# Performance work log

Measured on AMD Instinct MI355X. Metric: run time of the kernel, lower is better.

Reference implementation:

```python
import jax, jax.numpy as jnp
import numpy as np
from functools import partial

DIM, HID, DK, NH, SEQ, B = 1024, 512, 512, 4, 16, 2048
DH = DK // NH  # per-head dim = 128
EPS = 1e-5


def _ln(x, g, b):
    m = x.mean(-1, keepdims=True)
    v = ((x - m) ** 2).mean(-1, keepdims=True)
    return (x - m) * jax.lax.rsqrt(v + EPS) * g + b


def setup_inputs() -> dict:
    key = jax.random.key(0)
    ks = jax.random.split(key, 32)
    it = iter(range(32))
    n = lambda shape, s: jax.random.normal(ks[next(it)], shape, jnp.float32) * s
    inp = {
        'visual': n((B, SEQ, DIM), 1.0),
        'text':   n((B, SEQ, DIM), 1.0),
        'user':   n((B, SEQ, DIM), 1.0),
        'cat':    n((B, SEQ, DIM), 1.0),
        'label':  n((B, SEQ, 1), 1.0),
        'h0':     n((B, HID), 1.0),
        'c0':     n((B, HID), 1.0),
        # fusion MLP: Linear(4*dim -> dim)
        'fus_W': n((DIM, 4 * DIM), 1.0 / np.sqrt(4 * DIM)),
        'fus_b': n((DIM,), 0.01),
        # LayerNormLSTM cell params (gate order i,f,g,o)
        'W_ih': n((4 * HID, DIM), 1.0 / np.sqrt(DIM)),
        'W_hh': n((4 * HID, HID), 1.0 / np.sqrt(HID)),
        'g_ih': 1.0 + n((4 * HID,), 0.1), 'b_ih': n((4 * HID,), 0.01),
        'g_hh': 1.0 + n((4 * HID,), 0.1), 'b_hh': n((4 * HID,), 0.01),
        'g_c':  1.0 + n((HID,), 0.1),     'b_c':  n((HID,), 0.01),
        # attention projections
        'wq_W': n((DK, HID), 1.0 / np.sqrt(HID)), 'wq_b': n((DK,), 0.01),
        'wk_W': n((DK, HID), 1.0 / np.sqrt(HID)), 'wk_b': n((DK,), 0.01),
        'wv_W': n((NH, DK, HID), 1.0 / np.sqrt(HID)), 'wv_b': n((NH, DK), 0.01),
        'wout_W': n((DK, DK * NH), 1.0 / np.sqrt(DK * NH)), 'wout_b': n((DK,), 0.01),
        'out_W': n((1, DK), 1.0 / np.sqrt(DK)), 'out_b': n((1,), 0.01),
    }
    return inp


def reference(visual, text, user, cat, label, h0, c0, fus_W, fus_b,
              W_ih, W_hh, g_ih, b_ih, g_hh, b_hh, g_c, b_c,
              wq_W, wq_b, wk_W, wk_b, wv_W, wv_b, wout_W, wout_b, out_W, out_b):
    # fusion MLP (dropout is identity at inference)
    mods = jnp.concatenate([visual, text, user, cat], axis=-1)  # [B,S,4*DIM]
    v_t = jax.nn.relu(mods @ fus_W.T + fus_b)                    # [B,S,DIM]

    # LayerNorm-LSTM recurrence over time via scan
    def step(carry, x_t):
        h, c = carry
        gates = _ln(x_t @ W_ih.T, g_ih, b_ih) + _ln(h @ W_hh.T, g_hh, b_hh)
        i, f, g, o = jnp.split(gates, 4, axis=-1)
        c = jax.nn.sigmoid(f) * c + jax.nn.sigmoid(i) * jnp.tanh(g)
        h = jax.nn.sigmoid(o) * jnp.tanh(_ln(c, g_c, b_c))
        return (h, c), h

    (hn, _), hs = jax.lax.scan(step, (h0, c0), jnp.swapaxes(v_t, 0, 1))
    lstm_out = jnp.swapaxes(hs, 0, 1)  # [B,S,HID]

    # multi-head dot self-attention against final hidden state
    q = (hn @ wq_W.T + wq_b).reshape(-1, NH, DH)                    # [B,H,dh]
    k = (lstm_out @ wk_W.T + wk_b).reshape(-1, SEQ, NH, DH)         # [B,S,H,dh]
    scores = jnp.einsum('bshd,bhd->bhs', k, q) / np.sqrt(DH)        # [B,H,S]
    attn = jax.nn.softmax(scores, axis=-1)
    # per-head full-width values: V[b,h,s,k]
    V = jnp.einsum('hkd,bsd->bhsk', wv_W, lstm_out) + wv_b[None, :, None, :]
    ctx = jnp.einsum('bhsk,bhs->bhk', V, attn).reshape(-1, NH * DK)  # [B,H*DK]
    out_h = ctx @ wout_W.T + wout_b                                  # [B,DK]
    output = out_h @ out_W.T + out_b                                 # [B,1]

    label_one = label[:, -1, 0]
    loss = jnp.mean((output.reshape(-1) - label_one) ** 2)
    return loss, output
```

## Files before the change

### kernel.cpp

```cpp
#include <hip/hip_runtime.h>
#include <cstdint>

#define B_SZ 2048
#define SEQ  16
#define DIM  1024
#define HID  512
#define DK   512
#define NH   4
#define DH   128
#define GATE 2048
#define EPSV 1e-5f

typedef __bf16 bf8_t __attribute__((ext_vector_type(8)));
typedef float  f4_t  __attribute__((ext_vector_type(4)));
typedef unsigned short u16x8 __attribute__((ext_vector_type(8)));
typedef unsigned short u16x4 __attribute__((ext_vector_type(4)));

__device__ __forceinline__ unsigned short f2bf(float f){
  __bf16 h = (__bf16)f;
  return __builtin_bit_cast(unsigned short, h);
}
__device__ __forceinline__ float bf2f(unsigned short u){
  return __builtin_bit_cast(float, ((unsigned int)u) << 16);
}
__device__ __forceinline__ float sigm(float x){ return 1.f/(1.f+__expf(-x)); }
__device__ __forceinline__ float tanh_f(float x){ return 1.f - 2.f/(__expf(2.f*x)+1.f); }

__device__ __forceinline__ void gload16(const void* g, void* l){
  __builtin_amdgcn_global_load_lds(
      (const __attribute__((address_space(1))) void*)g,
      (__attribute__((address_space(3))) void*)l, 16, 0, 0);
}

template<bool OUT_BF16, bool BIAS, bool RELU>
__global__ __launch_bounds__(512, 1) void gemm8p(
    const unsigned short* __restrict__ A,
    const unsigned short* __restrict__ Bw,
    const float* __restrict__ bias,
    void* __restrict__ Cp,
    int N, int K, int nwg)
{
  __shared__ __align__(16) unsigned short As[2][256*64];
  __shared__ __align__(16) unsigned short Bs[2][256*64];
  const int tid = threadIdx.x, lane = tid & 63, w = tid >> 6;
  const int bid = blockIdx.x;
  const int swz = (bid & 7)*(nwg >> 3) + (bid >> 3);
  const int nx  = N >> 8;
  const int lnx = 31 - __clz(nx);
  const int bm0 = (swz >> lnx) << 8;
  const int bn0 = (swz & (nx-1)) << 8;

  const int l8  = lane >> 3;
  const int gsw = (lane & 7) ^ l8;
  const int fr  = lane & 15, kg = lane >> 4;
  const int wm  = (w >> 2)*128, wn = (w & 3)*64;
  const int KT  = K >> 6;

  auto stA = [&](int buf, int kt, int h){
    #pragma unroll
    for (int c=0;c<2;++c){
      const int rb = h*128 + c*64 + w*8;
      gload16(A + (size_t)(bm0 + rb + l8)*K + (size_t)kt*64 + gsw*8, &As[buf][rb*64]);
    }
  };
  auto stB = [&](int buf, int kt, int h){
    #pragma unroll
    for (int c=0;c<2;++c){
      const int rb = h*128 + c*64 + w*8;
      gload16(Bw + (size_t)(bn0 + rb + l8)*K + (size_t)kt*64 + gsw*8, &Bs[buf][rb*64]);
    }
  };
  auto rdA = [&](int buf, int m, int kk)->bf8_t{
    return *(const bf8_t*)&As[buf][(wm + m*16 + fr)*64 + (((kk*4+kg) ^ (fr&7))*8)];
  };
  auto rdB = [&](int buf, int n, int kk)->bf8_t{
    return *(const bf8_t*)&Bs[buf][(wn + n*16 + fr)*64 + (((kk*4+kg) ^ (fr&7))*8)];
  };

  f4_t acc[8][4];
  #pragma unroll
  for (int m=0;m<8;++m)
    #pragma unroll
    for (int n=0;n<4;++n) acc[m][n] = (f4_t)0.f;

  bf8_t bfr[4][2];

  auto mfma2 = [&](int m0, const bf8_t a00, const bf8_t a01,
                   const bf8_t a10, const bf8_t a11){
    __builtin_amdgcn_s_setprio(1);
    #pragma unroll
    for (int n=0;n<4;++n){
      acc[m0][n]   = __builtin_amdgcn_mfma_f32_16x16x32_bf16(a00, bfr[n][0], acc[m0][n],   0,0,0);
      acc[m0][n]   = __builtin_amdgcn_mfma_f32_16x16x32_bf16(a01, bfr[n][1], acc[m0][n],   0,0,0);
      acc[m0+1][n] = __builtin_amdgcn_mfma_f32_16x16x32_bf16(a10, bfr[n][0], acc[m0+1][n], 0,0,0);
      acc[m0+1][n] = __builtin_amdgcn_mfma_f32_16x16x32_bf16(a11, bfr[n][1], acc[m0+1][n], 0,0,0);
    }
    __builtin_amdgcn_s_setprio(0);
  };

  auto phase12 = [&](int buf, auto&& stg){
    #pragma unroll
    for (int n=0;n<4;++n){ bfr[n][0]=rdB(buf,n,0); bfr[n][1]=rdB(buf,n,1); }
    const bf8_t a00=rdA(buf,0,0), a01=rdA(buf,0,1), a10=rdA(buf,1,0), a11=rdA(buf,1,1);
    stg();
    asm volatile("s_barrier" ::: "memory");
    mfma2(0, a00,a01,a10,a11);
    asm volatile("s_barrier" ::: "memory");
  };
  auto phase4 = [&](int buf, int m0, auto&& stg, bool vm){
    const bf8_t a00=rdA(buf,m0,0), a01=rdA(buf,m0,1), a10=rdA(buf,m0+1,0), a11=rdA(buf,m0+1,1);
    stg();
    if (vm){
      __builtin_amdgcn_sched_barrier(0);
      asm volatile("s_waitcnt vmcnt(4)" ::: "memory");
    }
    asm volatile("s_barrier" ::: "memory");
    mfma2(m0, a00,a01,a10,a11);
    asm volatile("s_barrier" ::: "memory");
  };

  stA(0,0,0); stA(0,0,1); stB(0,0,0); stB(0,0,1);
  stB(1,1,0); stB(1,1,1);
  __builtin_amdgcn_sched_barrier(0);
  asm volatile("s_waitcnt vmcnt(4)" ::: "memory");
  asm volatile("s_barrier" ::: "memory");

  const int NIT = KT >> 1;
  for (int it=0; it<NIT; ++it){
    const int t0 = 2*it, t1 = t0+1;
    const int tN  = (t0+2 < KT) ? t0+2 : KT-1;
    const int tB3 = (t1+2 < KT) ? t1+2 : KT-1;

    phase12(0,      [&]{ stA(1,t1,0);  });
    phase4 (0, 2,   [&]{ stA(1,t1,1);  }, false);
    phase4 (0, 4,   [&]{ stB(0,tN,0);  }, false);
    phase4 (0, 6,   [&]{ stB(0,tN,1);  }, true);
    phase12(1,      [&]{ stA(0,tN,0);  });
    phase4 (1, 2,   [&]{ stA(0,tN,1);  }, false);
    phase4 (1, 4,   [&]{ stB(1,tB3,0); }, false);
    phase4 (1, 6,   [&]{ stB(1,tB3,1); }, true);
  }

  #pragma unroll
  for (int n=0;n<4;++n){
    const int col = bn0 + wn + n*16 + fr;
    float bv = 0.f;
    if constexpr (BIAS) bv = bias[col];
    #pragma unroll
    for (int m=0;m<8;++m){
      #pragma unroll
      for (int j=0;j<4;++j){
        const int row = bm0 + wm + m*16 + kg*4 + j;
        float v = acc[m][n][j] + bv;
        if constexpr (RELU) v = fmaxf(v, 0.f);
        if constexpr (OUT_BF16) ((unsigned short*)Cp)[(size_t)row*N + col] = f2bf(v);
        else                    ((float*)Cp)[(size_t)row*N + col] = v;
      }
    }
  }
}

__global__ __launch_bounds__(512, 1) void gemm8pf(
    const float* __restrict__ A0, const float* __restrict__ A1,
    const float* __restrict__ A2, const float* __restrict__ A3,
    const unsigned short* __restrict__ Bw,
    const float* __restrict__ bias,
    unsigned short* __restrict__ Cp,
    int N, int K, int nwg)
{
  __shared__ __align__(16) unsigned short As[2][256*64];
  __shared__ __align__(16) unsigned short Bs[2][256*64];
  const int tid = threadIdx.x, lane = tid & 63, w = tid >> 6;
  const int bid = blockIdx.x;
  const int swz = (bid & 7)*(nwg >> 3) + (bid >> 3);
  const int nx  = N >> 8;
  const int lnx = 31 - __clz(nx);
  const int bm0 = (swz >> lnx) << 8;
  const int bn0 = (swz & (nx-1)) << 8;

  const int l8  = lane >> 3;
  const int gsw = (lane & 7) ^ l8;
  const int fr  = lane & 15, kg = lane >> 4;
  const int wm  = (w >> 2)*128, wn = (w & 3)*64;
  const int KT  = K >> 6;

  auto stB = [&](int buf, int kt, int h){
    #pragma unroll
    for (int c=0;c<2;++c){
      const int rb = h*128 + c*64 + w*8;
      gload16(Bw + (size_t)(bn0 + rb + l8)*K + (size_t)kt*64 + gsw*8, &Bs[buf][rb*64]);
    }
  };

  f4_t rg0[2], rg1[2], rg2[2], rg3[2];
  auto ldQ = [&](f4_t* rg, int kt, int q){
    const int kb = kt*64, si = kb >> 10, kc = kb & 1023;
    const float* Asel = si==0?A0 : si==1?A1 : si==2?A2 : A3;
    const float* p = Asel + (size_t)(bm0 + q*64 + (tid>>3))*1024 + kc + (tid&7)*8;
    rg[0] = *(const f4_t*)p; rg[1] = *(const f4_t*)(p+4);
  };
  auto wrQ = [&](const f4_t* rg, int buf, int q){
    const int R = q*64 + (tid>>3);
    const int g = (tid&7) ^ (R&7);
    u16x8 wv;
    #pragma unroll
    for (int j=0;j<4;++j){ wv[j]=f2bf(rg[0][j]); wv[4+j]=f2bf(rg[1][j]); }
    *(u16x8*)&As[buf][R*64 + g*8] = wv;
  };

  auto rdA = [&](int buf, int m, int kk)->bf8_t{
    return *(const bf8_t*)&As[buf][(wm + m*16 + fr)*64 + (((kk*4+kg) ^ (fr&7))*8)];
  };
  auto rdB = [&](int buf, int n, int kk)->bf8_t{
    return *(const bf8_t*)&Bs[buf][(wn + n*16 + fr)*64 + (((kk*4+kg) ^ (fr&7))*8)];
  };

  f4_t acc[8][4];
  #pragma unroll
  for (int m=0;m<8;++m)
    #pragma unroll
    for (int n=0;n<4;++n) acc[m][n] = (f4_t)0.f;

  bf8_t bfr[4][2];

  auto mfma2 = [&](int m0, const bf8_t a00, const bf8_t a01,
                   const bf8_t a10, const bf8_t a11){
    __builtin_amdgcn_s_setprio(1);
    #pragma unroll
    for (int n=0;n<4;++n){
      acc[m0][n]   = __builtin_amdgcn_mfma_f32_16x16x32_bf16(a00, bfr[n][0], acc[m0][n],   0,0,0);
      acc[m0][n]   = __builtin_amdgcn_mfma_f32_16x16x32_bf16(a01, bfr[n][1], acc[m0][n],   0,0,0);
      acc[m0+1][n] = __builtin_amdgcn_mfma_f32_16x16x32_bf16(a10, bfr[n][0], acc[m0+1][n], 0,0,0);
      acc[m0+1][n] = __builtin_amdgcn_mfma_f32_16x16x32_bf16(a11, bfr[n][1], acc[m0+1][n], 0,0,0);
    }
    __builtin_amdgcn_s_setprio(0);
  };

  auto phase12 = [&](int buf, auto&& stg){
    #pragma unroll
    for (int n=0;n<4;++n){ bfr[n][0]=rdB(buf,n,0); bfr[n][1]=rdB(buf,n,1); }
    const bf8_t a00=rdA(buf,0,0), a01=rdA(buf,0,1), a10=rdA(buf,1,0), a11=rdA(buf,1,1);
    stg();
    asm volatile("s_barrier" ::: "memory");
    mfma2(0, a00,a01,a10,a11);
    asm volatile("s_barrier" ::: "memory");
  };
  auto phase4 = [&](int buf, int m0, auto&& stg){
    const bf8_t a00=rdA(buf,m0,0), a01=rdA(buf,m0,1), a10=rdA(buf,m0+1,0), a11=rdA(buf,m0+1,1);
    stg();
    asm volatile("s_barrier" ::: "memory");
    mfma2(m0, a00,a01,a10,a11);
    asm volatile("s_barrier" ::: "memory");
  };

  stB(0,0,0); stB(0,0,1); stB(1,1,0); stB(1,1,1);
  ldQ(rg0,0,0); ldQ(rg1,0,1); ldQ(rg2,0,2); ldQ(rg3,0,3);
  wrQ(rg0,0,0); wrQ(rg1,0,1); wrQ(rg2,0,2); wrQ(rg3,0,3);
  __builtin_amdgcn_sched_barrier(0);
  ldQ(rg0,1,0); ldQ(rg1,1,1); ldQ(rg2,1,2); ldQ(rg3,1,3);
  asm volatile("s_waitcnt lgkmcnt(0)" ::: "memory");
  asm volatile("s_barrier" ::: "memory");

  const int NIT = KT >> 1;
  for (int it=0; it<NIT; ++it){
    const int t1  = 2*it+1;
    const int tN  = (t1+1 < KT) ? t1+1 : KT-1;
    const int tB3 = (t1+2 < KT) ? t1+2 : KT-1;

    phase12(0, [&]{ wrQ(rg0,1,0); __builtin_amdgcn_sched_barrier(0); ldQ(rg0,tN,0); });
    phase4 (0, 2, [&]{ wrQ(rg1,1,1); __builtin_amdgcn_sched_barrier(0); ldQ(rg1,tN,1); });
    phase4 (0, 4, [&]{ wrQ(rg2,1,2); stB(0,tN,0);
                       __builtin_amdgcn_sched_barrier(0); ldQ(rg2,tN,2); });
    phase4 (0, 6, [&]{ wrQ(rg3,1,3); stB(0,tN,1);
                       __builtin_amdgcn_sched_barrier(0); ldQ(rg3,tN,3);
                       __builtin_amdgcn_sched_barrier(0);
                       asm volatile("s_waitcnt lgkmcnt(0)":::"memory"); });
    phase12(1, [&]{ wrQ(rg0,0,0); __builtin_amdgcn_sched_barrier(0); ldQ(rg0,tB3,0); });
    phase4 (1, 2, [&]{ wrQ(rg1,0,1); __builtin_amdgcn_sched_barrier(0); ldQ(rg1,tB3,1); });
    phase4 (1, 4, [&]{ wrQ(rg2,0,2); stB(1,tB3,0);
                       __builtin_amdgcn_sched_barrier(0); ldQ(rg2,tB3,2); });
    phase4 (1, 6, [&]{ wrQ(rg3,0,3); stB(1,tB3,1);
                       __builtin_amdgcn_sched_barrier(0); ldQ(rg3,tB3,3);
                       __builtin_amdgcn_sched_barrier(0);
                       asm volatile("s_waitcnt lgkmcnt(0)":::"memory"); });
  }

  #pragma unroll
  for (int n=0;n<4;++n){
    const int col = bn0 + wn + n*16 + fr;
    const float bv = bias[col];
    #pragma unroll
    for (int m=0;m<8;++m){
      #pragma unroll
      for (int j=0;j<4;++j){
        const int row = bm0 + wm + m*16 + kg*4 + j;
        float v = fmaxf(acc[m][n][j] + bv, 0.f);
        Cp[(size_t)row*N + col] = f2bf(v);
      }
    }
  }
}

template<bool OUT_BF16, bool BIAS>
__global__ __launch_bounds__(256) void gemm64(
    const unsigned short* __restrict__ A,
    const unsigned short* __restrict__ Bw,
    const float* __restrict__ bias,
    void* __restrict__ Cp,
    int N, int K, int nwg)
{
  __shared__ __align__(16) unsigned short As[64*64];
  __shared__ __align__(16) unsigned short Bs[64*64];
  const int tid = threadIdx.x, lane = tid & 63, wave = tid >> 6;
  const int bid = blockIdx.x;
  const int swz = (bid & 7)*(nwg >> 3) + (bid >> 3);
  const int nx  = N >> 6;
  const int lnx = 31 - __clz(nx);
  const int bm0 = (swz >> lnx) << 6;
  const int bn0 = (swz & (nx-1)) << 6;

  const int r8  = lane >> 3;
  const int gsw = ((lane & 7) ^ r8) * 8;
  const unsigned short* Ab = A  + (size_t)(bm0 + wave*16 + r8)*K + gsw;
  const unsigned short* Bb = Bw + (size_t)(bn0 + wave*16 + r8)*K + gsw;
  unsigned short* la = As + wave*1024;
  unsigned short* lb = Bs + wave*1024;

  f4_t acc[2][2];
  #pragma unroll
  for (int m=0;m<2;++m)
    #pragma unroll
    for (int n=0;n<2;++n) acc[m][n] = (f4_t)0.f;

  const int KT = K >> 6;
  const int fr = lane & 15, kg = lane >> 4;
  const int wm = (wave & 1)*32, wn = (wave >> 1)*32;

  for (int kt = 0; kt < KT; ++kt){
    if (kt) __syncthreads();
    const size_t ko = (size_t)kt*64;
    #pragma unroll
    for (int q = 0; q < 2; ++q){
      gload16(Ab + ko + (size_t)q*8*K, la + q*512);
      gload16(Bb + ko + (size_t)q*8*K, lb + q*512);
    }
    __syncthreads();
    #pragma unroll
    for (int kk = 0; kk < 2; ++kk){
      bf8_t af[2], bf_[2];
      #pragma unroll
      for (int m=0;m<2;++m){
        const int r = wm+m*16+fr;
        af[m]  = *(const bf8_t*)&As[r*64 + (((kk*4+kg) ^ (r&7))*8)];
      }
      #pragma unroll
      for (int n=0;n<2;++n){
        const int r = wn+n*16+fr;
        bf_[n] = *(const bf8_t*)&Bs[r*64 + (((kk*4+kg) ^ (r&7))*8)];
      }
      #pragma unroll
      for (int m=0;m<2;++m)
        #pragma unroll
        for (int n=0;n<2;++n)
          acc[m][n] = __builtin_amdgcn_mfma_f32_16x16x32_bf16(af[m], bf_[n], acc[m][n], 0,0,0);
    }
  }

  #pragma unroll
  for (int n=0;n<2;++n){
    const int col = bn0 + wn + n*16 + fr;
    float bv = 0.f;
    if constexpr (BIAS) bv = bias[col];
    #pragma unroll
    for (int m=0;m<2;++m){
      #pragma unroll
      for (int j=0;j<4;++j){
        const int row = bm0 + wm + m*16 + kg*4 + j;
        float v = acc[m][n][j] + bv;
        if constexpr (OUT_BF16) ((unsigned short*)Cp)[(size_t)row*N + col] = f2bf(v);
        else                    ((float*)Cp)[(size_t)row*N + col] = v;
      }
    }
  }
}

__global__ __launch_bounds__(256) void lstm_step(
  const unsigned short* __restrict__ X, const unsigned short* __restrict__ Gh,
  const float* __restrict__ c_src, float* __restrict__ c_dst,
  const float* __restrict__ g_ih, const float* __restrict__ b_ih,
  const float* __restrict__ g_hh, const float* __restrict__ b_hh,
  const float* __restrict__ g_c,  const float* __restrict__ b_c,
  unsigned short* __restrict__ h_out, unsigned short* __restrict__ lstm_out,
  int t)
{
  const int b = blockIdx.x, tid = threadIdx.x;
  __shared__ float xs[GATE];
  __shared__ float gs[GATE];
  __shared__ float red[32];
  const unsigned short* xrow = X  + ((size_t)b*SEQ + t)*GATE;
  const unsigned short* grow = Gh + (size_t)b*GATE;
  u16x8 xv = *(const u16x8*)&xrow[tid*8];
  u16x8 gv = *(const u16x8*)&grow[tid*8];
  float sx=0,sx2=0,sg=0,sg2=0;
  #pragma unroll
  for (int j=0;j<8;++j){
    float x = bf2f(xv[j]), g = bf2f(gv[j]);
    xs[tid*8+j]=x; gs[tid*8+j]=g;
    sx += x; sx2 += x*x; sg += g; sg2 += g*g;
  }
  #pragma unroll
  for (int m=32;m;m>>=1){
    sx += __shfl_xor(sx,m); sx2 += __shfl_xor(sx2,m);
    sg += __shfl_xor(sg,m); sg2 += __shfl_xor(sg2,m);
  }
  const int w = tid>>6;
  if ((tid&63)==0){ red[w]=sx; red[4+w]=sx2; red[8+w]=sg; red[12+w]=sg2; }
  __syncthreads();
  sx  = red[0]+red[1]+red[2]+red[3];
  sx2 = red[4]+red[5]+red[6]+red[7];
  sg  = red[8]+red[9]+red[10]+red[11];
  sg2 = red[12]+red[13]+red[14]+red[15];
  const float mX = sx*(1.f/GATE), mH = sg*(1.f/GATE);
  const float rX = rsqrtf(sx2*(1.f/GATE)-mX*mX+EPSV);
  const float rH = rsqrtf(sg2*(1.f/GATE)-mH*mH+EPSV);

  float cN[2], xo[2]; float sc=0, sc2=0;
  #pragma unroll
  for (int rep=0;rep<2;++rep){
    const int n = tid + rep*256;
    const int ni=n, nf=n+HID, ng=n+2*HID, no=n+3*HID;
    float gi = (xs[ni]-mX)*rX*g_ih[ni]+b_ih[ni] + (gs[ni]-mH)*rH*g_hh[ni]+b_hh[ni];
    float gf = (xs[nf]-mX)*rX*g_ih[nf]+b_ih[nf] + (gs[nf]-mH)*rH*g_hh[nf]+b_hh[nf];
    float gg = (xs[ng]-mX)*rX*g_ih[ng]+b_ih[ng] + (gs[ng]-mH)*rH*g_hh[ng]+b_hh[ng];
    float go = (xs[no]-mX)*rX*g_ih[no]+b_ih[no] + (gs[no]-mH)*rH*g_hh[no]+b_hh[no];
    float co = c_src[(size_t)b*HID + n];
    float cn = sigm(gf)*co + sigm(gi)*tanh_f(gg);
    cN[rep]=cn; xo[rep]=go;
    sc += cn; sc2 += cn*cn;
  }
  #pragma unroll
  for (int m=32;m;m>>=1){ sc += __shfl_xor(sc,m); sc2 += __shfl_xor(sc2,m); }
  if ((tid&63)==0){ red[16+w]=sc; red[20+w]=sc2; }
  __syncthreads();
  sc  = red[16]+red[17]+red[18]+red[19];
  sc2 = red[20]+red[21]+red[22]+red[23];
  const float mC = sc*(1.f/HID);
  const float rC = rsqrtf(sc2*(1.f/HID)-mC*mC+EPSV);
  #pragma unroll
  for (int rep=0;rep<2;++rep){
    const int n = tid + rep*256;
    float hN = sigm(xo[rep])*tanh_f((cN[rep]-mC)*rC*g_c[n]+b_c[n]);
    c_dst[(size_t)b*HID+n] = cN[rep];
    unsigned short hbv = f2bf(hN);
    h_out[(size_t)b*HID+n] = hbv;
    lstm_out[((size_t)b*SEQ+t)*HID+n] = hbv;
  }
}

__global__ __launch_bounds__(256) void attn_out_k(
  const float* __restrict__ q, const unsigned short* __restrict__ Km,
  const unsigned short* __restrict__ lo_all,
  const float* __restrict__ u, const float* __restrict__ Cc,
  float* __restrict__ out)
{
  const int b = blockIdx.x, tid = threadIdx.x;
  __shared__ float qs[DK];
  __shared__ float sc[NH][SEQ];
  __shared__ float at[NH][SEQ];
  __shared__ float red[4];
  for (int i=tid; i<DK; i+=256) qs[i] = q[(size_t)b*DK + i];
  __syncthreads();
  {
    const int p = tid>>2, sub = tid&3, h = p>>4, s = p&15;
    const unsigned short* krow = Km + ((size_t)b*SEQ + s)*DK + h*DH + sub*32;
    const float* qh = &qs[h*DH + sub*32];
    float part = 0.f;
    #pragma unroll
    for (int c8=0;c8<4;++c8){
      u16x8 kv = *(const u16x8*)(krow + c8*8);
      #pragma unroll
      for (int j=0;j<8;++j) part += qh[c8*8+j]*bf2f(kv[j]);
    }
    part += __shfl_xor(part,1); part += __shfl_xor(part,2);
    if (sub==0) sc[h][s] = part * 0.08838834764831845f;
  }
  __syncthreads();
  if (tid < 64){
    const int h = tid>>4;
    float v = sc[h][tid&15], mx = v;
    #pragma unroll
    for (int m=1;m<16;m<<=1) mx = fmaxf(mx, __shfl_xor(mx,m));
    float e = __expf(v-mx), se = e;
    #pragma unroll
    for (int m=1;m<16;m<<=1) se += __shfl_xor(se,m);
    at[h][tid&15] = e/se;
  }
  __syncthreads();
  float accum = 0.f;
  #pragma unroll
  for (int it=0; it<4; ++it){
    const int idx = it*256 + tid;
    const int h = idx>>8, d0 = (idx&255)*2;
    const unsigned short* lo = lo_all + (size_t)b*SEQ*HID + d0;
    float p0=0.f, p1=0.f;
    #pragma unroll
    for (int s=0;s<16;++s){
      unsigned int pr = *(const unsigned int*)(lo + s*HID);
      float a = at[h][s];
      p0 += a*bf2f((unsigned short)(pr&0xffffu));
      p1 += a*bf2f((unsigned short)(pr>>16));
    }
    accum += u[h*HID+d0]*p0 + u[h*HID+d0+1]*p1;
  }
  #pragma unroll
  for (int m=32;m;m>>=1) accum += __shfl_xor(accum,m);
  if ((tid&63)==0) red[tid>>6] = accum;
  __syncthreads();
  if (tid==0) out[1+b] = red[0]+red[1]+red[2]+red[3] + Cc[0];
}

__global__ __launch_bounds__(256) void loss_k(const float* __restrict__ label, float* __restrict__ out){
  const int tid = threadIdx.x;
  __shared__ float red[4];
  float s = 0.f;
  for (int b=tid; b<B_SZ; b+=256){
    float d = out[1+b] - label[(size_t)b*SEQ + (SEQ-1)];
    s += d*d;
  }
  #pragma unroll
  for (int m=32;m;m>>=1) s += __shfl_xor(s,m);
  if ((tid&63)==0) red[tid>>6]=s;
  __syncthreads();
  if (tid==0) out[0] = (red[0]+red[1]+red[2]+red[3]) * (1.f/B_SZ);
}

__global__ __launch_bounds__(256) void cvt_bf16_k(const float* __restrict__ in, unsigned short* __restrict__ o, int n){
  int i = (blockIdx.x*256 + threadIdx.x)*4;
  if (i < n){
    f4_t v = *(const f4_t*)&in[i];
    u16x4 w;
    #pragma unroll
    for (int j=0;j<4;++j) w[j] = f2bf(v[j]);
    *(u16x4*)&o[i] = w;
  }
}

__global__ __launch_bounds__(256) void fold_we_k(
  const float* __restrict__ wout_W, const float* __restrict__ out_W, float* __restrict__ we)
{
  const int j = blockIdx.x*256 + threadIdx.x;
  float s=0.f;
  for (int m=0;m<512;++m) s += out_W[m]*wout_W[(size_t)m*2048+j];
  we[j]=s;
}
__global__ __launch_bounds__(256) void fold_u_k(
  const float* __restrict__ we, const float* __restrict__ wv_W, float* __restrict__ u)
{
  const int o = blockIdx.x*256 + threadIdx.x;
  const int h = o>>9, d = o&511;
  const float* wv = wv_W + (size_t)h*262144 + d;
  const float* wp = we + h*512;
  float s=0.f;
  for (int k=0;k<512;++k) s += wp[k]*wv[(size_t)k*512];
  u[o]=s;
}
__global__ __launch_bounds__(256) void fold_c_k(
  const float* __restrict__ we, const float* __restrict__ wv_b,
  const float* __restrict__ out_W, const float* __restrict__ wout_b,
  const float* __restrict__ out_b, float* __restrict__ Cc)
{
  const int tid = threadIdx.x;
  __shared__ float red[4];
  float s=0.f;
  for (int j=tid;j<2048;j+=256) s += we[j]*wv_b[j];
  for (int m=tid;m<512;m+=256)  s += out_W[m]*wout_b[m];
  #pragma unroll
  for (int m=32;m;m>>=1) s += __shfl_xor(s,m);
  if ((tid&63)==0) red[tid>>6]=s;
  __syncthreads();
  if (tid==0) Cc[0] = red[0]+red[1]+red[2]+red[3] + out_b[0];
}

extern "C" void kernel_launch(void* const* d_in, const int* in_sizes, int n_in,
                              void* d_out, int out_size, void* d_ws, size_t ws_size,
                              hipStream_t stream)
{
  const float* visual = (const float*)d_in[0];
  const float* text   = (const float*)d_in[1];
  const float* user_  = (const float*)d_in[2];
  const float* cat_   = (const float*)d_in[3];
  const float* label  = (const float*)d_in[4];
  const float* h0     = (const float*)d_in[5];
  const float* c0     = (const float*)d_in[6];
  const float* fus_W  = (const float*)d_in[7];
  const float* fus_b  = (const float*)d_in[8];
  const float* W_ih   = (const float*)d_in[9];
  const float* W_hh   = (const float*)d_in[10];
  const float* g_ih   = (const float*)d_in[11];
  const float* b_ih   = (const float*)d_in[12];
  const float* g_hh   = (const float*)d_in[13];
  const float* b_hh   = (const float*)d_in[14];
  const float* g_c    = (const float*)d_in[15];
  const float* b_c    = (const float*)d_in[16];
  const float* wq_W   = (const float*)d_in[17];
  const float* wq_b   = (const float*)d_in[18];
  const float* wk_W   = (const float*)d_in[19];
  const float* wk_b   = (const float*)d_in[20];
  const float* wv_W   = (const float*)d_in[21];
  const float* wv_b   = (const float*)d_in[22];
  const float* wout_W = (const float*)d_in[23];
  const float* wout_b = (const float*)d_in[24];
  const float* out_W  = (const float*)d_in[25];
  const float* out_b  = (const float*)d_in[26];
  (void)in_sizes; (void)n_in; (void)out_size; (void)ws_size;

  char* base = (char*)d_ws; size_t off = 0;
  auto alloc = [&](size_t n)->void*{ void* p = base+off; off += n; off = (off+255)&~(size_t)255; return p; };
  unsigned short* X     = (unsigned short*)alloc((size_t)32768*2048*2);
  unsigned short* vt    = (unsigned short*)alloc((size_t)32768*1024*2);
  unsigned short* lo    = (unsigned short*)alloc((size_t)32768*512*2);
  unsigned short* Km    = (unsigned short*)alloc((size_t)32768*512*2);
  unsigned short* Gh    = (unsigned short*)alloc((size_t)2048*2048*2);
  float*          cws   = (float*)         alloc((size_t)2048*512*4);
  unsigned short* hb    = (unsigned short*)alloc((size_t)2048*512*2);
  float*          qb    = (float*)         alloc((size_t)2048*512*4);
  unsigned short* fusWb = (unsigned short*)alloc((size_t)1024*4096*2);
  unsigned short* Wihb  = (unsigned short*)alloc((size_t)2048*1024*2);
  unsigned short* Whhb  = (unsigned short*)alloc((size_t)2048*512*2);
  unsigned short* wqb   = (unsigned short*)alloc((size_t)512*512*2);
  unsigned short* wkb   = (unsigned short*)alloc((size_t)512*512*2);
  float*          we_ws = (float*)         alloc(2048*4);
  float*          u_ws  = (float*)         alloc(2048*4);
  float*          C_ws  = (float*)         alloc(256);

  cvt_bf16_k<<<dim3(4096), dim3(256), 0, stream>>>(fus_W, fusWb, 1024*4096);
  cvt_bf16_k<<<dim3(2048), dim3(256), 0, stream>>>(W_ih,  Wihb,  2048*1024);
  cvt_bf16_k<<<dim3(1024), dim3(256), 0, stream>>>(W_hh,  Whhb,  2048*512);
  cvt_bf16_k<<<dim3(256),  dim3(256), 0, stream>>>(wq_W,  wqb,   512*512);
  cvt_bf16_k<<<dim3(256),  dim3(256), 0, stream>>>(wk_W,  wkb,   512*512);
  cvt_bf16_k<<<dim3(1024), dim3(256), 0, stream>>>(h0,    hb,    2048*512);
  fold_we_k<<<dim3(8), dim3(256), 0, stream>>>(wout_W, out_W, we_ws);
  fold_u_k <<<dim3(8), dim3(256), 0, stream>>>(we_ws, wv_W, u_ws);
  fold_c_k <<<dim3(1), dim3(256), 0, stream>>>(we_ws, wv_b, out_W, wout_b, out_b, C_ws);

  gemm8pf<<<dim3(512), dim3(512), 0, stream>>>(
      visual, text, user_, cat_, fusWb, fus_b, vt, 1024, 4096, 512);
  gemm8p<true,false,false><<<dim3(1024), dim3(512), 0, stream>>>(
      vt, Wihb, nullptr, X, 2048, 1024, 1024);

  for (int t=0; t<SEQ; ++t){
    gemm64<true,false><<<dim3(1024), dim3(256), 0, stream>>>(
        hb, Whhb, nullptr, Gh, 2048, 512, 1024);
    lstm_step<<<dim3(2048), dim3(256), 0, stream>>>(
        X, Gh, (t==0 ? c0 : cws), cws, g_ih, b_ih, g_hh, b_hh, g_c, b_c, hb, lo, t);
  }

  gemm64<false,true><<<dim3(256), dim3(256), 0, stream>>>(
      hb, wqb, wq_b, qb, 512, 512, 256);
  gemm8p<true,true,false><<<dim3(256), dim3(512), 0, stream>>>(
      lo, wkb, wk_b, Km, 512, 512, 256);

  attn_out_k<<<dim3(2048), dim3(256), 0, stream>>>(qb, Km, lo, u_ws, C_ws, (float*)d_out);
  loss_k<<<dim3(1), dim3(256), 0, stream>>>(label, (float*)d_out);
}
```

Baseline: 933.2 us.

## Fold key projection into query side and batch LSTM rows per block

The full key projection over every timestep is replaced by projecting each head's query through the key weights. A small block-masked GEMM produces per-batch qk vectors, and scores become dot products directly against the LSTM outputs. The key bias is dropped because it adds the same constant to every timestep's score, and softmax ignores that. The attention kernel now stages LSTM outputs in shared memory once and reuses them for both scores and context. lstm_step handles four batch rows per block and keeps the gain and bias parameters in registers. The query is also stored as bf16, which adds a little rounding error.

```diff
diff --git a/kernel.cpp b/kernel.cpp
--- a/kernel.cpp
+++ b/kernel.cpp
@@ -10,6 +10,7 @@
 #define DH   128
 #define GATE 2048
 #define EPSV 1e-5f
+#define LOP  520
 
 typedef __bf16 bf8_t __attribute__((ext_vector_type(8)));
 typedef float  f4_t  __attribute__((ext_vector_type(4)));
@@ -301,6 +302,90 @@
   }
 }
 
+template<bool OUT_BF16, bool BIAS, bool RELU>
+__global__ __launch_bounds__(256) void gemm16(
+    const unsigned short* __restrict__ A,
+    const unsigned short* __restrict__ Bw,
+    const float* __restrict__ bias,
+    void* __restrict__ Cp,
+    int N, int K, int nwg)
+{
+  __shared__ __align__(16) unsigned short As[128*64];
+  __shared__ __align__(16) unsigned short Bs[128*64];
+  const int tid = threadIdx.x, lane = tid & 63, wave = tid >> 6;
+  const int bid = blockIdx.x;
+  const int swz = (bid & 7)*(nwg >> 3) + (bid >> 3);
+  const int nx  = N >> 7;
+  const int lnx = 31 - __clz(nx);
+  const int bm0 = (swz >> lnx) << 7;
+  const int bn0 = (swz & (nx-1)) << 7;
+
+  const int r8  = lane >> 3;
+  const int gsw = ((lane & 7) ^ r8) * 8;
+  const unsigned short* Ab = A  + (size_t)(bm0 + wave*32 + r8)*K + gsw;
+  const unsigned short* Bb = Bw + (size_t)(bn0 + wave*32 + r8)*K + gsw;
+  unsigned short* la = As + wave*2048;
+  unsigned short* lb = Bs + wave*2048;
+
+  f4_t acc[4][4];
+  #pragma unroll
+  for (int m=0;m<4;++m)
+    #pragma unroll
+    for (int n=0;n<4;++n) acc[m][n] = (f4_t)0.f;
+
+  const int KT = K >> 6;
+  const int fr = lane & 15, kg = lane >> 4;
+  const int wm = (wave & 1)*64, wn = (wave >> 1)*64;
+
+  for (int kt = 0; kt < KT; ++kt){
+    if (kt) __syncthreads();
+    const size_t ko = (size_t)kt*64;
+    #pragma unroll
+    for (int q = 0; q < 4; ++q){
+      gload16(Ab + ko + (size_t)q*8*K, la + q*512);
+      gload16(Bb + ko + (size_t)q*8*K, lb + q*512);
+    }
+    __syncthreads();
+    #pragma unroll
+    for (int kk = 0; kk < 2; ++kk){
+      bf8_t af[4], bf_[4];
+      #pragma unroll
+      for (int m=0;m<4;++m){
+        const int r = wm+m*16+fr;
+        af[m]  = *(const bf8_t*)&As[r*64 + (((kk*4+kg) ^ (r&7))*8)];
+      }
+      #pragma unroll
+      for (int n=0;n<4;++n){
+        const int r = wn+n*16+fr;
+        bf_[n] = *(const bf8_t*)&Bs[r*64 + (((kk*4+kg) ^ (r&7))*8)];
+      }
+      #pragma unroll
+      for (int m=0;m<4;++m)
+        #pragma unroll
+        for (int n=0;n<4;++n)
+          acc[m][n] = __builtin_amdgcn_mfma_f32_16x16x32_bf16(af[m], bf_[n], acc[m][n], 0,0,0);
+    }
+  }
+
+  #pragma unroll
+  for (int n=0;n<4;++n){
+    const int col = bn0 + wn + n*16 + fr;
+    float bv = 0.f;
+    if constexpr (BIAS) bv = bias[col];
+    #pragma unroll
+    for (int m=0;m<4;++m){
+      #pragma unroll
+      for (int j=0;j<4;++j){
+        const int row = bm0 + wm + m*16 + kg*4 + j;
+        float v = acc[m][n][j] + bv;
+        if constexpr (RELU) v = fmaxf(v, 0.f);
+        if constexpr (OUT_BF16) ((unsigned short*)Cp)[(size_t)row*N + col] = f2bf(v);
+        else                    ((float*)Cp)[(size_t)row*N + col] = v;
+      }
+    }
+  }
+}
+
 template<bool OUT_BF16, bool BIAS>
 __global__ __launch_bounds__(256) void gemm64(
     const unsigned short* __restrict__ A,
@@ -393,93 +478,129 @@
   unsigned short* __restrict__ h_out, unsigned short* __restrict__ lstm_out,
   int t)
 {
-  const int b = blockIdx.x, tid = threadIdx.x;
+  const int tid = threadIdx.x;
   __shared__ float xs[GATE];
   __shared__ float gs[GATE];
   __shared__ float red[32];
-  const unsigned short* xrow = X  + ((size_t)b*SEQ + t)*GATE;
-  const unsigned short* grow = Gh + (size_t)b*GATE;
-  u16x8 xv = *(const u16x8*)&xrow[tid*8];
-  u16x8 gv = *(const u16x8*)&grow[tid*8];
-  float sx=0,sx2=0,sg=0,sg2=0;
-  #pragma unroll
-  for (int j=0;j<8;++j){
-    float x = bf2f(xv[j]), g = bf2f(gv[j]);
-    xs[tid*8+j]=x; gs[tid*8+j]=g;
-    sx += x; sx2 += x*x; sg += g; sg2 += g*g;
-  }
-  #pragma unroll
-  for (int m=32;m;m>>=1){
-    sx += __shfl_xor(sx,m); sx2 += __shfl_xor(sx2,m);
-    sg += __shfl_xor(sg,m); sg2 += __shfl_xor(sg2,m);
-  }
-  const int w = tid>>6;
-  if ((tid&63)==0){ red[w]=sx; red[4+w]=sx2; red[8+w]=sg; red[12+w]=sg2; }
-  __syncthreads();
-  sx  = red[0]+red[1]+red[2]+red[3];
-  sx2 = red[4]+red[5]+red[6]+red[7];
-  sg  = red[8]+red[9]+red[10]+red[11];
-  sg2 = red[12]+red[13]+red[14]+red[15];
-  const float mX = sx*(1.f/GATE), mH = sg*(1.f/GATE);
-  const float rX = rsqrtf(sx2*(1.f/GATE)-mX*mX+EPSV);
-  const float rH = rsqrtf(sg2*(1.f/GATE)-mH*mH+EPSV);
-
-  float cN[2], xo[2]; float sc=0, sc2=0;
+
+  float Wgi[2][4], Wbi[2][4], Wgh[2][4], Wbh[2][4], Wgc[2], Wbc[2];
   #pragma unroll
   for (int rep=0;rep<2;++rep){
     const int n = tid + rep*256;
-    const int ni=n, nf=n+HID, ng=n+2*HID, no=n+3*HID;
-    float gi = (xs[ni]-mX)*rX*g_ih[ni]+b_ih[ni] + (gs[ni]-mH)*rH*g_hh[ni]+b_hh[ni];
-    float gf = (xs[nf]-mX)*rX*g_ih[nf]+b_ih[nf] + (gs[nf]-mH)*rH*g_hh[nf]+b_hh[nf];
-    float gg = (xs[ng]-mX)*rX*g_ih[ng]+b_ih[ng] + (gs[ng]-mH)*rH*g_hh[ng]+b_hh[ng];
-    float go = (xs[no]-mX)*rX*g_ih[no]+b_ih[no] + (gs[no]-mH)*rH*g_hh[no]+b_hh[no];
-    float co = c_src[(size_t)b*HID + n];
-    float cn = sigm(gf)*co + sigm(gi)*tanh_f(gg);
-    cN[rep]=cn; xo[rep]=go;
-    sc += cn; sc2 += cn*cn;
-  }
-  #pragma unroll
-  for (int m=32;m;m>>=1){ sc += __shfl_xor(sc,m); sc2 += __shfl_xor(sc2,m); }
-  if ((tid&63)==0){ red[16+w]=sc; red[20+w]=sc2; }
-  __syncthreads();
-  sc  = red[16]+red[17]+red[18]+red[19];
-  sc2 = red[20]+red[21]+red[22]+red[23];
-  const float mC = sc*(1.f/HID);
-  const float rC = rsqrtf(sc2*(1.f/HID)-mC*mC+EPSV);
-  #pragma unroll
-  for (int rep=0;rep<2;++rep){
-    const int n = tid + rep*256;
-    float hN = sigm(xo[rep])*tanh_f((cN[rep]-mC)*rC*g_c[n]+b_c[n]);
-    c_dst[(size_t)b*HID+n] = cN[rep];
-    unsigned short hbv = f2bf(hN);
-    h_out[(size_t)b*HID+n] = hbv;
-    lstm_out[((size_t)b*SEQ+t)*HID+n] = hbv;
-  }
+    #pragma unroll
+    for (int g=0;g<4;++g){
+      Wgi[rep][g]=g_ih[n+g*HID]; Wbi[rep][g]=b_ih[n+g*HID];
+      Wgh[rep][g]=g_hh[n+g*HID]; Wbh[rep][g]=b_hh[n+g*HID];
+    }
+    Wgc[rep]=g_c[n]; Wbc[rep]=b_c[n];
+  }
+
+  for (int rr=0; rr<4; ++rr){
+    const int b = blockIdx.x*4 + rr;
+    const unsigned short* xrow = X  + ((size_t)b*SEQ + t)*GATE;
+    const unsigned short* grow = Gh + (size_t)b*GATE;
+    u16x8 xv = *(const u16x8*)&xrow[tid*8];
+    u16x8 gv = *(const u16x8*)&grow[tid*8];
+    float sx=0,sx2=0,sg=0,sg2=0;
+    #pragma unroll
+    for (int j=0;j<8;++j){
+      float x = bf2f(xv[j]), g = bf2f(gv[j]);
+      xs[tid*8+j]=x; gs[tid*8+j]=g;
+      sx += x; sx2 += x*x; sg += g; sg2 += g*g;
+    }
+    #pragma unroll
+    for (int m=32;m;m>>=1){
+      sx += __shfl_xor(sx,m); sx2 += __shfl_xor(sx2,m);
+      sg += __shfl_xor(sg,m); sg2 += __shfl_xor(sg2,m);
+    }
+    const int w = tid>>6;
+    if ((tid&63)==0){ red[w]=sx; red[4+w]=sx2; red[8+w]=sg; red[12+w]=sg2; }
+    __syncthreads();
+    sx  = red[0]+red[1]+red[2]+red[3];
+    sx2 = red[4]+red[5]+red[6]+red[7];
+    sg  = red[8]+red[9]+red[10]+red[11];
+    sg2 = red[12]+red[13]+red[14]+red[15];
+    const float mX = sx*(1.f/GATE), mH = sg*(1.f/GATE);
+    const float rX = rsqrtf(sx2*(1.f/GATE)-mX*mX+EPSV);
+    const float rH = rsqrtf(sg2*(1.f/GATE)-mH*mH+EPSV);
+
+    float cN[2], xo[2]; float sc=0, sc2=0;
+    #pragma unroll
+    for (int rep=0;rep<2;++rep){
+      const int n = tid + rep*256;
+      const int ni=n, nf=n+HID, ng=n+2*HID, no=n+3*HID;
+      float gi = (xs[ni]-mX)*rX*Wgi[rep][0]+Wbi[rep][0] + (gs[ni]-mH)*rH*Wgh[rep][0]+Wbh[rep][0];
+      float gf = (xs[nf]-mX)*rX*Wgi[rep][1]+Wbi[rep][1] + (gs[nf]-mH)*rH*Wgh[rep][1]+Wbh[rep][1];
+      float gg = (xs[ng]-mX)*rX*Wgi[rep][2]+Wbi[rep][2] + (gs[ng]-mH)*rH*Wgh[rep][2]+Wbh[rep][2];
+      float go = (xs[no]-mX)*rX*Wgi[rep][3]+Wbi[rep][3] + (gs[no]-mH)*rH*Wgh[rep][3]+Wbh[rep][3];
+      float co = c_src[(size_t)b*HID + n];
+      float cn = sigm(gf)*co + sigm(gi)*tanh_f(gg);
+      cN[rep]=cn; xo[rep]=go;
+      sc += cn; sc2 += cn*cn;
+    }
+    #pragma unroll
+    for (int m=32;m;m>>=1){ sc += __shfl_xor(sc,m); sc2 += __shfl_xor(sc2,m); }
+    if ((tid&63)==0){ red[16+w]=sc; red[20+w]=sc2; }
+    __syncthreads();
+    sc  = red[16]+red[17]+red[18]+red[19];
+    sc2 = red[20]+red[21]+red[22]+red[23];
+    const float mC = sc*(1.f/HID);
+    const float rC = rsqrtf(sc2*(1.f/HID)-mC*mC+EPSV);
+    #pragma unroll
+    for (int rep=0;rep<2;++rep){
+      const int n = tid + rep*256;
+      float hN = sigm(xo[rep])*tanh_f((cN[rep]-mC)*rC*Wgc[rep]+Wbc[rep]);
+      c_dst[(size_t)b*HID+n] = cN[rep];
+      unsigned short hbv = f2bf(hN);
+      h_out[(size_t)b*HID+n] = hbv;
+      lstm_out[((size_t)b*SEQ+t)*HID+n] = hbv;
+    }
+    __syncthreads();
+  }
+}
+
+__global__ __launch_bounds__(256) void wk2_k(const float* __restrict__ wk_W,
+                                             unsigned short* __restrict__ WK2){
+  const int idx = blockIdx.x*256 + threadIdx.x;
+  const int r = idx >> 9, k = idx & 511;
+  float v = ((k>>7) == (r>>9)) ? wk_W[(size_t)k*512 + (r&511)] : 0.f;
+  WK2[idx] = f2bf(v);
 }
 
 __global__ __launch_bounds__(256) void attn_out_k(
-  const float* __restrict__ q, const unsigned short* __restrict__ Km,
+  const float* __restrict__ qk,
   const unsigned short* __restrict__ lo_all,
   const float* __restrict__ u, const float* __restrict__ Cc,
   float* __restrict__ out)
 {
   const int b = blockIdx.x, tid = threadIdx.x;
-  __shared__ float qs[DK];
+  __shared__ unsigned short lo_s[SEQ*LOP];
+  __shared__ float qk_s[4*HID];
   __shared__ float sc[NH][SEQ];
   __shared__ float at[NH][SEQ];
   __shared__ float red[4];
-  for (int i=tid; i<DK; i+=256) qs[i] = q[(size_t)b*DK + i];
+  {
+    const unsigned short* lp = lo_all + (size_t)b*SEQ*HID;
+    const int r = tid>>4, c0 = (tid&15)*32;
+    #pragma unroll
+    for (int e=0;e<4;++e)
+      *(u16x8*)&lo_s[r*LOP + c0 + e*8] = *(const u16x8*)&lp[r*HID + c0 + e*8];
+    const float* qp = qk + (size_t)b*2048;
+    #pragma unroll
+    for (int e=0;e<2;++e)
+      *(f4_t*)&qk_s[tid*4 + e*1024] = *(const f4_t*)&qp[tid*4 + e*1024];
+  }
   __syncthreads();
   {
     const int p = tid>>2, sub = tid&3, h = p>>4, s = p&15;
-    const unsigned short* krow = Km + ((size_t)b*SEQ + s)*DK + h*DH + sub*32;
-    const float* qh = &qs[h*DH + sub*32];
+    const float* qh = &qk_s[h*HID + sub*128];
+    const unsigned short* lrow = &lo_s[s*LOP + sub*128];
     float part = 0.f;
     #pragma unroll
-    for (int c8=0;c8<4;++c8){
-      u16x8 kv = *(const u16x8*)(krow + c8*8);
-      #pragma unroll
-      for (int j=0;j<8;++j) part += qh[c8*8+j]*bf2f(kv[j]);
+    for (int j=0;j<128;j+=8){
+      u16x8 lv = *(const u16x8*)(lrow + j);
+      #pragma unroll
+      for (int e=0;e<8;++e) part += qh[j+e]*bf2f(lv[e]);
     }
     part += __shfl_xor(part,1); part += __shfl_xor(part,2);
     if (sub==0) sc[h][s] = part * 0.08838834764831845f;
@@ -501,11 +622,10 @@
   for (int it=0; it<4; ++it){
     const int idx = it*256 + tid;
     const int h = idx>>8, d0 = (idx&255)*2;
-    const unsigned short* lo = lo_all + (size_t)b*SEQ*HID + d0;
     float p0=0.f, p1=0.f;
     #pragma unroll
     for (int s=0;s<16;++s){
-      unsigned int pr = *(const unsigned int*)(lo + s*HID);
+      unsigned int pr = *(const unsigned int*)&lo_s[s*LOP + d0];
       float a = at[h][s];
       p0 += a*bf2f((unsigned short)(pr&0xffffu));
       p1 += a*bf2f((unsigned short)(pr>>16));
@@ -612,23 +732,23 @@
   const float* wout_b = (const float*)d_in[24];
   const float* out_W  = (const float*)d_in[25];
   const float* out_b  = (const float*)d_in[26];
-  (void)in_sizes; (void)n_in; (void)out_size; (void)ws_size;
+  (void)in_sizes; (void)n_in; (void)out_size; (void)ws_size; (void)wk_b;
 
   char* base = (char*)d_ws; size_t off = 0;
   auto alloc = [&](size_t n)->void*{ void* p = base+off; off += n; off = (off+255)&~(size_t)255; return p; };
   unsigned short* X     = (unsigned short*)alloc((size_t)32768*2048*2);
   unsigned short* vt    = (unsigned short*)alloc((size_t)32768*1024*2);
   unsigned short* lo    = (unsigned short*)alloc((size_t)32768*512*2);
-  unsigned short* Km    = (unsigned short*)alloc((size_t)32768*512*2);
+  float*          qk    = (float*)         alloc((size_t)2048*2048*4);
   unsigned short* Gh    = (unsigned short*)alloc((size_t)2048*2048*2);
   float*          cws   = (float*)         alloc((size_t)2048*512*4);
   unsigned short* hb    = (unsigned short*)alloc((size_t)2048*512*2);
-  float*          qb    = (float*)         alloc((size_t)2048*512*4);
+  unsigned short* qb    = (unsigned short*)alloc((size_t)2048*512*2);
   unsigned short* fusWb = (unsigned short*)alloc((size_t)1024*4096*2);
   unsigned short* Wihb  = (unsigned short*)alloc((size_t)2048*1024*2);
   unsigned short* Whhb  = (unsigned short*)alloc((size_t)2048*512*2);
   unsigned short* wqb   = (unsigned short*)alloc((size_t)512*512*2);
-  unsigned short* wkb   = (unsigned short*)alloc((size_t)512*512*2);
+  unsigned short* WK2   = (unsigned short*)alloc((size_t)2048*512*2);
   float*          we_ws = (float*)         alloc(2048*4);
   float*          u_ws  = (float*)         alloc(2048*4);
   float*          C_ws  = (float*)         alloc(256);
@@ -637,8 +757,8 @@
   cvt_bf16_k<<<dim3(2048), dim3(256), 0, stream>>>(W_ih,  Wihb,  2048*1024);
   cvt_bf16_k<<<dim3(1024), dim3(256), 0, stream>>>(W_hh,  Whhb,  2048*512);
   cvt_bf16_k<<<dim3(256),  dim3(256), 0, stream>>>(wq_W,  wqb,   512*512);
-  cvt_bf16_k<<<dim3(256),  dim3(256), 0, stream>>>(wk_W,  wkb,   512*512);
   cvt_bf16_k<<<dim3(1024), dim3(256), 0, stream>>>(h0,    hb,    2048*512);
+  wk2_k<<<dim3(4096), dim3(256), 0, stream>>>(wk_W, WK2);
   fold_we_k<<<dim3(8), dim3(256), 0, stream>>>(wout_W, out_W, we_ws);
   fold_u_k <<<dim3(8), dim3(256), 0, stream>>>(we_ws, wv_W, u_ws);
   fold_c_k <<<dim3(1), dim3(256), 0, stream>>>(we_ws, wv_b, out_W, wout_b, out_b, C_ws);
@@ -651,15 +771,15 @@
   for (int t=0; t<SEQ; ++t){
     gemm64<true,false><<<dim3(1024), dim3(256), 0, stream>>>(
         hb, Whhb, nullptr, Gh, 2048, 512, 1024);
-    lstm_step<<<dim3(2048), dim3(256), 0, stream>>>(
+    lstm_step<<<dim3(512), dim3(256), 0, stream>>>(
         X, Gh, (t==0 ? c0 : cws), cws, g_ih, b_ih, g_hh, b_hh, g_c, b_c, hb, lo, t);
   }
 
-  gemm64<false,true><<<dim3(256), dim3(256), 0, stream>>>(
+  gemm64<true,true><<<dim3(256), dim3(256), 0, stream>>>(
       hb, wqb, wq_b, qb, 512, 512, 256);
-  gemm8p<true,true,false><<<dim3(256), dim3(512), 0, stream>>>(
-      lo, wkb, wk_b, Km, 512, 512, 256);
-
-  attn_out_k<<<dim3(2048), dim3(256), 0, stream>>>(qb, Km, lo, u_ws, C_ws, (float*)d_out);
+  gemm16<false,false,false><<<dim3(256), dim3(256), 0, stream>>>(
+      qb, WK2, nullptr, qk, 2048, 512, 256);
+
+  attn_out_k<<<dim3(2048), dim3(256), 0, stream>>>(qk, lo, u_ws, C_ws, (float*)d_out);
   loss_k<<<dim3(1), dim3(256), 0, stream>>>(label, (float*)d_out);
 }
```

Measured after the change: 988.6 us. +5.9%, slower.
